# Kernel tuning notes

Measured on AMD Instinct MI355X. Metric: run time of the kernel, lower is better.

## Reference

```python
import jax, jax.numpy as jnp
import numpy as np

B, S, E, H = 4, 2048, 512, 8
D = E // H


def setup_inputs() -> dict:
    key = jax.random.key(0)
    ks = jax.random.split(key, 12)
    sc = 0.02
    return {
        "x": jax.random.normal(ks[0], (B, S, E), jnp.float32),
        "edge_bias": jax.random.normal(ks[1], (B, S, S), jnp.float32),
        "attn_mask": jax.random.randint(ks[2], (B, 1, S, S), 0, 2, jnp.int32),
        "Wq": jax.random.normal(ks[3], (E, E), jnp.float32) * sc,
        "bq": jnp.zeros((E,), jnp.float32),
        "Wk": jax.random.normal(ks[4], (E, E), jnp.float32) * sc,
        "bk": jnp.zeros((E,), jnp.float32),
        "Wv": jax.random.normal(ks[5], (E, E), jnp.float32) * sc,
        "bv": jnp.zeros((E,), jnp.float32),
        "Wo": jax.random.normal(ks[6], (E, E), jnp.float32) * sc,
        "bo": jnp.zeros((E,), jnp.float32),
    }


def reference(x, edge_bias, attn_mask, Wq, bq, Wk, bk, Wv, bv, Wo, bo):
    scale = D ** -0.5
    # projections -> [B, H, S, D]
    def proj(W, b):
        return (x @ W.T + b).reshape(B, S, H, D).transpose(0, 2, 1, 3)
    q = proj(Wq, bq)
    k = proj(Wk, bk)
    v = proj(Wv, bv)
    # scores [B, H, S, S] with edge bias and mask before softmax
    scores = jnp.einsum("bhqd,bhkd->bhqk", q, k) * scale
    scores = scores + edge_bias[:, None, :, :]
    scores = jnp.where(attn_mask == 0, -jnp.inf, scores)
    probs = jax.nn.softmax(scores, axis=-1)
    out = jnp.einsum("bhqk,bhkd->bhqd", probs, v)
    out = out.transpose(0, 2, 1, 3).reshape(B, S, E)
    return out @ Wo.T + bo
```

## Files before the change

### kernel.cpp

```cpp
#include <hip/hip_runtime.h>
#include <hip/hip_bf16.h>
#include <stdint.h>

#define DEV static __device__ __forceinline__

typedef float f32x4 __attribute__((ext_vector_type(4)));
typedef int   i32x4 __attribute__((ext_vector_type(4)));
typedef unsigned short u16x4 __attribute__((ext_vector_type(4)));
typedef unsigned u32x2 __attribute__((ext_vector_type(2)));
typedef unsigned u32x4 __attribute__((ext_vector_type(4)));
typedef __bf16 bf16x8 __attribute__((ext_vector_type(8)));

constexpr int Bb = 4, Ss = 2048, Ee = 512, Hh = 8, Dd = 64;
constexpr float LOG2E = 1.4426950408889634f;

DEV unsigned short f2bf(float f) {
  unsigned u = __float_as_uint(f);
  u += 0x7fff + ((u >> 16) & 1);
  return (unsigned short)(u >> 16);
}

DEV unsigned cvtpk(float lo, float hi) {
  unsigned r;
  asm("v_cvt_pk_bf16_f32 %0, %1, %2" : "=v"(r) : "v"(lo), "v"(hi));
  return r;
}

DEV void gload16(const void* g, void* l) {
  __builtin_amdgcn_global_load_lds((__attribute__((address_space(1))) void*)(g),
                                   (__attribute__((address_space(3))) void*)(l), 16, 0, 0);
}

__global__ void k_cvt(const float* __restrict__ src, unsigned short* __restrict__ dst, int n4) {
  int i = blockIdx.x * 256 + threadIdx.x;
  if (i >= n4) return;
  f32x4 v = *(const f32x4*)(src + (size_t)i * 4);
  u16x4 o;
#pragma unroll
  for (int j = 0; j < 4; ++j) o[j] = f2bf(v[j]);
  *(u16x4*)(dst + (size_t)i * 4) = o;
}

__global__ void k_mb(const float* __restrict__ bias, const int* __restrict__ mask,
                     unsigned short* __restrict__ mb, int n4) {
  int i = blockIdx.x * 256 + threadIdx.x;
  if (i >= n4) return;
  f32x4 v = *(const f32x4*)(bias + (size_t)i * 4);
  i32x4 m = *(const i32x4*)(mask + (size_t)i * 4);
  u16x4 o;
  const unsigned short NEG = f2bf(-1e38f * LOG2E);
#pragma unroll
  for (int j = 0; j < 4; ++j) o[j] = m[j] ? f2bf(v[j] * LOG2E) : NEG;
  *(u16x4*)(mb + (size_t)i * 4) = o;
}

template <int MODE>
__global__ __launch_bounds__(256) void k_gemm(
    const unsigned short* __restrict__ A, const unsigned short* __restrict__ Bw,
    const float* __restrict__ b0, const float* __restrict__ b1, const float* __restrict__ b2,
    unsigned short* __restrict__ oq, unsigned short* __restrict__ ok,
    unsigned short* __restrict__ ovt, float* __restrict__ of32) {
  __shared__ unsigned short Asl[128 * 32];
  __shared__ unsigned short Bsl[128 * 32];
  const int tid = threadIdx.x;
  const int wave = tid >> 6, lane = tid & 63;
  const int l15 = lane & 15, lg = lane >> 4;
  const int brow = blockIdx.x, bcol = blockIdx.y;
  const int wm = (wave >> 1) * 64, wn = (wave & 1) * 64;

  f32x4 acc[4][4] = {};

  for (int k0 = 0; k0 < 512; k0 += 32) {
    __syncthreads();
#pragma unroll
    for (int rnd = 0; rnd < 2; ++rnd) {
      int vid = rnd * 256 + tid;
      int r = vid >> 2, c = vid & 3;
      gload16(A + (size_t)(brow * 128 + r) * 512 + k0 + c * 8,
              Asl + (size_t)(rnd * 256 + wave * 64) * 8);
      gload16(Bw + (size_t)(bcol * 128 + r) * 512 + k0 + c * 8,
              Bsl + (size_t)(rnd * 256 + wave * 64) * 8);
    }
    __syncthreads();
    bf16x8 af[4], bfr[4];
#pragma unroll
    for (int m = 0; m < 4; ++m) af[m] = *(const bf16x8*)(Asl + (wm + m * 16 + l15) * 32 + lg * 8);
#pragma unroll
    for (int n = 0; n < 4; ++n) bfr[n] = *(const bf16x8*)(Bsl + (wn + n * 16 + l15) * 32 + lg * 8);
#pragma unroll
    for (int m = 0; m < 4; ++m)
#pragma unroll
      for (int n = 0; n < 4; ++n)
        acc[m][n] = __builtin_amdgcn_mfma_f32_16x16x32_bf16(af[m], bfr[n], acc[m][n], 0, 0, 0);
  }

  if (MODE == 0) {
    const int Nbase = bcol * 128;
    const int mat = Nbase >> 9;
    const int colb = Nbase & 511;
    const float* bp = (mat == 0) ? b0 : ((mat == 1) ? b1 : b2);
#pragma unroll
    for (int m = 0; m < 4; ++m)
#pragma unroll
      for (int n = 0; n < 4; ++n) {
        const int col = colb + wn + n * 16 + l15;
        const int h = col >> 6, d = col & 63;
        const float bv = bp[col];
#pragma unroll
        for (int j = 0; j < 4; ++j) {
          const int M = brow * 128 + wm + m * 16 + lg * 4 + j;
          const int b = M >> 11, s = M & 2047;
          float outv = acc[m][n][j] + bv;
          if (mat == 0) outv *= 0.125f * LOG2E;
          const unsigned short hv = f2bf(outv);
          if (mat == 0)
            oq[(((size_t)(b * Hh + h)) * Ss + s) * Dd + d] = hv;
          else if (mat == 1)
            ok[(((size_t)(b * Hh + h)) * Ss + s) * Dd + d] = hv;
          else
            ovt[(((size_t)(b * Hh + h)) * Dd + d) * Ss + s] = hv;
        }
      }
  } else {
#pragma unroll
    for (int m = 0; m < 4; ++m)
#pragma unroll
      for (int n = 0; n < 4; ++n) {
        const int col = bcol * 128 + wn + n * 16 + l15;
        const float bv = b0[col];
#pragma unroll
        for (int j = 0; j < 4; ++j) {
          const int M = brow * 128 + wm + m * 16 + lg * 4 + j;
          of32[(size_t)M * 512 + col] = acc[m][n][j] + bv;
        }
      }
  }
}

__global__ __launch_bounds__(256, 2) void k_attn(
    const unsigned short* __restrict__ q, const unsigned short* __restrict__ k,
    const unsigned short* __restrict__ vt, const unsigned short* __restrict__ mb,
    unsigned short* __restrict__ att) {
  __shared__ unsigned short Ksl[2][4096];
  __shared__ unsigned short Vsl[2][4096];
  __shared__ unsigned short Psl[4][2][1024];
  const int tid = threadIdx.x;
  const int wave = tid >> 6, lane = tid & 63;
  const int l15 = lane & 15, lg = lane >> 4;
  const int bid = blockIdx.x;
  const int xcd = bid & 7, slot = bid >> 3;
  const int bh = (xcd << 2) | (slot >> 4);
  const int qt = slot & 15;
  const int b = bh >> 3, h = bh & 7;
  const size_t qkb = (size_t)bh * Ss * Dd;
  const size_t vtbase = (size_t)bh * Dd * Ss;
  const int q0 = qt * 128 + wave * 32;

  const int swz = (l15 & 7) << 3;
  const int lgs8 = (lg ^ ((l15 >> 1) & 3)) * 8;

  bf16x8 qf[2][2];
#pragma unroll
  for (int g = 0; g < 2; ++g)
#pragma unroll
    for (int ks = 0; ks < 2; ++ks)
      qf[g][ks] = *(const bf16x8*)(q + qkb + (size_t)(q0 + g * 16 + l15) * Dd + ks * 32 + lg * 8);

  size_t mbrow[2];
#pragma unroll
  for (int g = 0; g < 2; ++g)
    mbrow[g] = ((size_t)b * Ss + (q0 + g * 16 + l15)) * Ss + lg * 4;

  const unsigned one2 = 0x3F803F80u;
  u32x4 ow; ow[0] = one2; ow[1] = one2; ow[2] = one2; ow[3] = one2;
  const bf16x8 onesv = __builtin_bit_cast(bf16x8, ow);

  f32x4 accO[2][4] = {};
  f32x4 accL[2] = {};

  {
#pragma unroll
    for (int rnd = 0; rnd < 2; ++rnd) {
      int v2 = rnd * 256 + tid;
      int ks = v2 >> 8, r = (v2 >> 2) & 63, c = v2 & 3;
      int cs = c ^ ((r >> 1) & 3);
      gload16(k + qkb + (size_t)r * Dd + ks * 32 + cs * 8,
              &Ksl[0][(rnd * 256 + wave * 64) * 8]);
    }
#pragma unroll
    for (int rnd = 0; rnd < 2; ++rnd) {
      int v2 = rnd * 256 + tid;
      int ks = v2 >> 8, r = (v2 >> 2) & 63, c = v2 & 3;
      int cs = c ^ ((r >> 1) & 3);
      gload16(vt + vtbase + (size_t)r * Ss + ks * 32 + cs * 8,
              &Vsl[0][(rnd * 256 + wave * 64) * 8]);
    }
  }
  u16x4 bvv[2][4];
#pragma unroll
  for (int g = 0; g < 2; ++g)
#pragma unroll
    for (int m = 0; m < 4; ++m)
      bvv[g][m] = *(const u16x4*)(mb + mbrow[g] + m * 16);

  for (int t = 0; t < 32; ++t) {
    const int cur = t & 1;
    __syncthreads();

    f32x4 binit[2][4];
#pragma unroll
    for (int g = 0; g < 2; ++g)
#pragma unroll
      for (int m = 0; m < 4; ++m)
#pragma unroll
        for (int j = 0; j < 4; ++j)
          binit[g][m][j] = __uint_as_float(((unsigned)bvv[g][m][j]) << 16);

    if (t < 31) {
      const int key0 = (t + 1) * 64;
#pragma unroll
      for (int rnd = 0; rnd < 2; ++rnd) {
        int v2 = rnd * 256 + tid;
        int ks = v2 >> 8, r = (v2 >> 2) & 63, c = v2 & 3;
        int cs = c ^ ((r >> 1) & 3);
        gload16(k + qkb + (size_t)(key0 + r) * Dd + ks * 32 + cs * 8,
                &Ksl[cur ^ 1][(rnd * 256 + wave * 64) * 8]);
      }
#pragma unroll
      for (int rnd = 0; rnd < 2; ++rnd) {
        int v2 = rnd * 256 + tid;
        int ks = v2 >> 8, r = (v2 >> 2) & 63, c = v2 & 3;
        int cs = c ^ ((r >> 1) & 3);
        gload16(vt + vtbase + (size_t)r * Ss + key0 + ks * 32 + cs * 8,
                &Vsl[cur ^ 1][(rnd * 256 + wave * 64) * 8]);
      }
#pragma unroll
      for (int g = 0; g < 2; ++g)
#pragma unroll
        for (int m = 0; m < 4; ++m)
          bvv[g][m] = *(const u16x4*)(mb + mbrow[g] + key0 + m * 16);
    }

    f32x4 sc[2][4];
    {
      bf16x8 kfm[4];
#pragma unroll
      for (int m = 0; m < 4; ++m)
        kfm[m] = *(const bf16x8*)(&Ksl[cur][(m * 16 + l15) * 32 + lgs8]);
      __builtin_amdgcn_s_setprio(1);
#pragma unroll
      for (int g = 0; g < 2; ++g)
#pragma unroll
        for (int m = 0; m < 4; ++m)
          sc[g][m] = __builtin_amdgcn_mfma_f32_16x16x32_bf16(kfm[m], qf[g][0], binit[g][m], 0, 0, 0);
      __builtin_amdgcn_s_setprio(0);
#pragma unroll
      for (int m = 0; m < 4; ++m)
        kfm[m] = *(const bf16x8*)(&Ksl[cur][2048 + (m * 16 + l15) * 32 + lgs8]);
      __builtin_amdgcn_s_setprio(1);
#pragma unroll
      for (int g = 0; g < 2; ++g)
#pragma unroll
        for (int m = 0; m < 4; ++m)
          sc[g][m] = __builtin_amdgcn_mfma_f32_16x16x32_bf16(kfm[m], qf[g][1], sc[g][m], 0, 0, 0);
      __builtin_amdgcn_s_setprio(0);
    }

#pragma unroll
    for (int m = 0; m < 4; ++m)
#pragma unroll
      for (int j = 0; j < 4; ++j) {
        sc[0][m][j] = exp2f(sc[0][m][j]);
        sc[1][m][j] = exp2f(sc[1][m][j]);
      }

#pragma unroll
    for (int g = 0; g < 2; ++g)
#pragma unroll
      for (int m = 0; m < 4; ++m) {
        u32x2 w;
        w[0] = cvtpk(sc[g][m][0], sc[g][m][1]);
        w[1] = cvtpk(sc[g][m][2], sc[g][m][3]);
        *(u32x2*)(&Psl[wave][g][(l15 * 64 + m * 16 + lg * 4) ^ swz]) = w;
      }
    asm volatile("" ::: "memory");

#pragma unroll
    for (int ks2 = 0; ks2 < 2; ++ks2) {
      bf16x8 va[4];
#pragma unroll
      for (int n = 0; n < 4; ++n)
        va[n] = *(const bf16x8*)(&Vsl[cur][ks2 * 2048 + (n * 16 + l15) * 32 + lgs8]);
      const bf16x8 pB0 = *(const bf16x8*)(&Psl[wave][0][(l15 * 64 + ks2 * 32 + lg * 8) ^ swz]);
      const bf16x8 pB1 = *(const bf16x8*)(&Psl[wave][1][(l15 * 64 + ks2 * 32 + lg * 8) ^ swz]);
      __builtin_amdgcn_s_setprio(1);
#pragma unroll
      for (int n = 0; n < 4; ++n) {
        accO[0][n] = __builtin_amdgcn_mfma_f32_16x16x32_bf16(va[n], pB0, accO[0][n], 0, 0, 0);
        accO[1][n] = __builtin_amdgcn_mfma_f32_16x16x32_bf16(va[n], pB1, accO[1][n], 0, 0, 0);
      }
      accL[0] = __builtin_amdgcn_mfma_f32_16x16x32_bf16(onesv, pB0, accL[0], 0, 0, 0);
      accL[1] = __builtin_amdgcn_mfma_f32_16x16x32_bf16(onesv, pB1, accL[1], 0, 0, 0);
      __builtin_amdgcn_s_setprio(0);
    }
  }

#pragma unroll
  for (int g = 0; g < 2; ++g) {
    const float invl = 1.0f / accL[g][0];
    const int qrow = q0 + g * 16 + l15;
#pragma unroll
    for (int n = 0; n < 4; ++n) {
      u16x4 o;
#pragma unroll
      for (int j = 0; j < 4; ++j) o[j] = f2bf(accO[g][n][j] * invl);
      *(u16x4*)(att + ((size_t)b * Ss + qrow) * Ee + h * Dd + n * 16 + lg * 4) = o;
    }
  }
}

extern "C" void kernel_launch(void* const* d_in, const int* in_sizes, int n_in,
                              void* d_out, int out_size, void* d_ws, size_t ws_size,
                              hipStream_t stream) {
  const float* x  = (const float*)d_in[0];
  const float* eb = (const float*)d_in[1];
  const int*   am = (const int*)d_in[2];
  const float* Wq = (const float*)d_in[3];
  const float* bq = (const float*)d_in[4];
  const float* Wk = (const float*)d_in[5];
  const float* bk = (const float*)d_in[6];
  const float* Wv = (const float*)d_in[7];
  const float* bv = (const float*)d_in[8];
  const float* Wo = (const float*)d_in[9];
  const float* bo = (const float*)d_in[10];
  float* out = (float*)d_out;

  unsigned short* xb   = (unsigned short*)d_ws;
  unsigned short* wqkv = xb + (size_t)8192 * 512;
  unsigned short* wo   = wqkv + (size_t)1536 * 512;
  unsigned short* qb   = wo + (size_t)512 * 512;
  unsigned short* kb   = qb + (size_t)Bb * Hh * Ss * Dd;
  unsigned short* vtb  = kb + (size_t)Bb * Hh * Ss * Dd;
  unsigned short* attb = vtb + (size_t)Bb * Hh * Ss * Dd;
  unsigned short* mbb  = attb + (size_t)8192 * 512;

  k_cvt<<<4096, 256, 0, stream>>>(x, xb, 8192 * 512 / 4);
  k_cvt<<<256, 256, 0, stream>>>(Wq, wqkv, 512 * 512 / 4);
  k_cvt<<<256, 256, 0, stream>>>(Wk, wqkv + (size_t)512 * 512, 512 * 512 / 4);
  k_cvt<<<256, 256, 0, stream>>>(Wv, wqkv + (size_t)1024 * 512, 512 * 512 / 4);
  k_cvt<<<256, 256, 0, stream>>>(Wo, wo, 512 * 512 / 4);
  k_mb<<<16384, 256, 0, stream>>>(eb, am, mbb, Bb * Ss * Ss / 4);

  dim3 blk(256);
  dim3 g1(64, 12);
  k_gemm<0><<<g1, blk, 0, stream>>>(xb, wqkv, bq, bk, bv, qb, kb, vtb, nullptr);
  k_attn<<<512, blk, 0, stream>>>(qb, kb, vtb, mbb, attb);
  dim3 g3(64, 4);
  k_gemm<1><<<g3, blk, 0, stream>>>(attb, wo, bo, nullptr, nullptr, nullptr, nullptr, nullptr, out);
}
```

Measured before the change: 165.2 us.

## Split attention over key halves with atomic fp32 reduction and separate normalize kernel

Attention blocks are doubled (1024) by splitting the key range into two halves per query tile. Partial unnormalized outputs and row sums go to fp32 workspace through atomics, and a new transpose/normalize kernel then writes the bf16 attention output. P staging in LDS is halved by processing the two query groups one after another, and launch bounds are raised to 4 blocks per CU for more occupancy. The cost is zeroing kernels, atomic traffic with a strided layout, and an extra pass over a 16MB fp32 buffer.

```diff
diff --git a/kernel.cpp b/kernel.cpp
--- a/kernel.cpp
+++ b/kernel.cpp
@@ -7,6 +7,7 @@
 typedef float f32x4 __attribute__((ext_vector_type(4)));
 typedef int   i32x4 __attribute__((ext_vector_type(4)));
 typedef unsigned short u16x4 __attribute__((ext_vector_type(4)));
+typedef unsigned short u16x8 __attribute__((ext_vector_type(8)));
 typedef unsigned u32x2 __attribute__((ext_vector_type(2)));
 typedef unsigned u32x4 __attribute__((ext_vector_type(4)));
 typedef __bf16 bf16x8 __attribute__((ext_vector_type(8)));
@@ -39,6 +40,13 @@
 #pragma unroll
   for (int j = 0; j < 4; ++j) o[j] = f2bf(v[j]);
   *(u16x4*)(dst + (size_t)i * 4) = o;
+}
+
+__global__ void k_zero(float* __restrict__ p, int n4) {
+  int i = blockIdx.x * 256 + threadIdx.x;
+  if (i >= n4) return;
+  f32x4 z = {};
+  *(f32x4*)(p + (size_t)i * 4) = z;
 }
 
 __global__ void k_mb(const float* __restrict__ bias, const int* __restrict__ mask,
@@ -137,24 +145,27 @@
   }
 }
 
-__global__ __launch_bounds__(256, 2) void k_attn(
+__global__ __launch_bounds__(256, 4) void k_attn(
     const unsigned short* __restrict__ q, const unsigned short* __restrict__ k,
     const unsigned short* __restrict__ vt, const unsigned short* __restrict__ mb,
-    unsigned short* __restrict__ att) {
+    float* __restrict__ accOf, float* __restrict__ accLf) {
   __shared__ unsigned short Ksl[2][4096];
   __shared__ unsigned short Vsl[2][4096];
-  __shared__ unsigned short Psl[4][2][1024];
+  __shared__ unsigned short Psl[4][1024];
   const int tid = threadIdx.x;
   const int wave = tid >> 6, lane = tid & 63;
   const int l15 = lane & 15, lg = lane >> 4;
   const int bid = blockIdx.x;
   const int xcd = bid & 7, slot = bid >> 3;
-  const int bh = (xcd << 2) | (slot >> 4);
-  const int qt = slot & 15;
+  const int bh = (xcd << 2) | (slot >> 5);
+  const int rem = slot & 31;
+  const int qt = rem >> 1;
+  const int ksp = rem & 1;
   const int b = bh >> 3, h = bh & 7;
   const size_t qkb = (size_t)bh * Ss * Dd;
   const size_t vtbase = (size_t)bh * Dd * Ss;
   const int q0 = qt * 128 + wave * 32;
+  const int kbase = ksp * 1024;
 
   const int swz = (l15 & 7) << 3;
   const int lgs8 = (lg ^ ((l15 >> 1) & 3)) * 8;
@@ -169,7 +180,7 @@
   size_t mbrow[2];
 #pragma unroll
   for (int g = 0; g < 2; ++g)
-    mbrow[g] = ((size_t)b * Ss + (q0 + g * 16 + l15)) * Ss + lg * 4;
+    mbrow[g] = ((size_t)b * Ss + (q0 + g * 16 + l15)) * Ss + lg * 4 + kbase;
 
   const unsigned one2 = 0x3F803F80u;
   u32x4 ow; ow[0] = one2; ow[1] = one2; ow[2] = one2; ow[3] = one2;
@@ -184,7 +195,7 @@
       int v2 = rnd * 256 + tid;
       int ks = v2 >> 8, r = (v2 >> 2) & 63, c = v2 & 3;
       int cs = c ^ ((r >> 1) & 3);
-      gload16(k + qkb + (size_t)r * Dd + ks * 32 + cs * 8,
+      gload16(k + qkb + (size_t)(kbase + r) * Dd + ks * 32 + cs * 8,
               &Ksl[0][(rnd * 256 + wave * 64) * 8]);
     }
 #pragma unroll
@@ -192,7 +203,7 @@
       int v2 = rnd * 256 + tid;
       int ks = v2 >> 8, r = (v2 >> 2) & 63, c = v2 & 3;
       int cs = c ^ ((r >> 1) & 3);
-      gload16(vt + vtbase + (size_t)r * Ss + ks * 32 + cs * 8,
+      gload16(vt + vtbase + (size_t)r * Ss + kbase + ks * 32 + cs * 8,
               &Vsl[0][(rnd * 256 + wave * 64) * 8]);
     }
   }
@@ -203,7 +214,7 @@
     for (int m = 0; m < 4; ++m)
       bvv[g][m] = *(const u16x4*)(mb + mbrow[g] + m * 16);
 
-  for (int t = 0; t < 32; ++t) {
+  for (int t = 0; t < 16; ++t) {
     const int cur = t & 1;
     __syncthreads();
 
@@ -216,8 +227,8 @@
         for (int j = 0; j < 4; ++j)
           binit[g][m][j] = __uint_as_float(((unsigned)bvv[g][m][j]) << 16);
 
-    if (t < 31) {
-      const int key0 = (t + 1) * 64;
+    if (t < 15) {
+      const int key0 = kbase + (t + 1) * 64;
 #pragma unroll
       for (int rnd = 0; rnd < 2; ++rnd) {
         int v2 = rnd * 256 + tid;
@@ -238,7 +249,7 @@
       for (int g = 0; g < 2; ++g)
 #pragma unroll
         for (int m = 0; m < 4; ++m)
-          bvv[g][m] = *(const u16x4*)(mb + mbrow[g] + key0 + m * 16);
+          bvv[g][m] = *(const u16x4*)(mb + mbrow[g] + (t + 1) * 64 + m * 16);
     }
 
     f32x4 sc[2][4];
@@ -274,48 +285,98 @@
         sc[1][m][j] = exp2f(sc[1][m][j]);
       }
 
-#pragma unroll
-    for (int g = 0; g < 2; ++g)
-#pragma unroll
-      for (int m = 0; m < 4; ++m) {
-        u32x2 w;
-        w[0] = cvtpk(sc[g][m][0], sc[g][m][1]);
-        w[1] = cvtpk(sc[g][m][2], sc[g][m][3]);
-        *(u32x2*)(&Psl[wave][g][(l15 * 64 + m * 16 + lg * 4) ^ swz]) = w;
-      }
+    bf16x8 va[2][4];
+#pragma unroll
+    for (int ks2 = 0; ks2 < 2; ++ks2)
+#pragma unroll
+      for (int n = 0; n < 4; ++n)
+        va[ks2][n] = *(const bf16x8*)(&Vsl[cur][ks2 * 2048 + (n * 16 + l15) * 32 + lgs8]);
+
+#pragma unroll
+    for (int m = 0; m < 4; ++m) {
+      u32x2 w;
+      w[0] = cvtpk(sc[0][m][0], sc[0][m][1]);
+      w[1] = cvtpk(sc[0][m][2], sc[0][m][3]);
+      *(u32x2*)(&Psl[wave][(l15 * 64 + m * 16 + lg * 4) ^ swz]) = w;
+    }
     asm volatile("" ::: "memory");
-
 #pragma unroll
     for (int ks2 = 0; ks2 < 2; ++ks2) {
-      bf16x8 va[4];
+      const bf16x8 pB = *(const bf16x8*)(&Psl[wave][(l15 * 64 + ks2 * 32 + lg * 8) ^ swz]);
+      __builtin_amdgcn_s_setprio(1);
 #pragma unroll
       for (int n = 0; n < 4; ++n)
-        va[n] = *(const bf16x8*)(&Vsl[cur][ks2 * 2048 + (n * 16 + l15) * 32 + lgs8]);
-      const bf16x8 pB0 = *(const bf16x8*)(&Psl[wave][0][(l15 * 64 + ks2 * 32 + lg * 8) ^ swz]);
-      const bf16x8 pB1 = *(const bf16x8*)(&Psl[wave][1][(l15 * 64 + ks2 * 32 + lg * 8) ^ swz]);
+        accO[0][n] = __builtin_amdgcn_mfma_f32_16x16x32_bf16(va[ks2][n], pB, accO[0][n], 0, 0, 0);
+      accL[0] = __builtin_amdgcn_mfma_f32_16x16x32_bf16(onesv, pB, accL[0], 0, 0, 0);
+      __builtin_amdgcn_s_setprio(0);
+    }
+    asm volatile("" ::: "memory");
+
+#pragma unroll
+    for (int m = 0; m < 4; ++m) {
+      u32x2 w;
+      w[0] = cvtpk(sc[1][m][0], sc[1][m][1]);
+      w[1] = cvtpk(sc[1][m][2], sc[1][m][3]);
+      *(u32x2*)(&Psl[wave][(l15 * 64 + m * 16 + lg * 4) ^ swz]) = w;
+    }
+    asm volatile("" ::: "memory");
+#pragma unroll
+    for (int ks2 = 0; ks2 < 2; ++ks2) {
+      const bf16x8 pB = *(const bf16x8*)(&Psl[wave][(l15 * 64 + ks2 * 32 + lg * 8) ^ swz]);
       __builtin_amdgcn_s_setprio(1);
 #pragma unroll
-      for (int n = 0; n < 4; ++n) {
-        accO[0][n] = __builtin_amdgcn_mfma_f32_16x16x32_bf16(va[n], pB0, accO[0][n], 0, 0, 0);
-        accO[1][n] = __builtin_amdgcn_mfma_f32_16x16x32_bf16(va[n], pB1, accO[1][n], 0, 0, 0);
-      }
-      accL[0] = __builtin_amdgcn_mfma_f32_16x16x32_bf16(onesv, pB0, accL[0], 0, 0, 0);
-      accL[1] = __builtin_amdgcn_mfma_f32_16x16x32_bf16(onesv, pB1, accL[1], 0, 0, 0);
+      for (int n = 0; n < 4; ++n)
+        accO[1][n] = __builtin_amdgcn_mfma_f32_16x16x32_bf16(va[ks2][n], pB, accO[1][n], 0, 0, 0);
+      accL[1] = __builtin_amdgcn_mfma_f32_16x16x32_bf16(onesv, pB, accL[1], 0, 0, 0);
       __builtin_amdgcn_s_setprio(0);
     }
   }
 
 #pragma unroll
   for (int g = 0; g < 2; ++g) {
-    const float invl = 1.0f / accL[g][0];
     const int qrow = q0 + g * 16 + l15;
 #pragma unroll
-    for (int n = 0; n < 4; ++n) {
-      u16x4 o;
-#pragma unroll
-      for (int j = 0; j < 4; ++j) o[j] = f2bf(accO[g][n][j] * invl);
-      *(u16x4*)(att + ((size_t)b * Ss + qrow) * Ee + h * Dd + n * 16 + lg * 4) = o;
-    }
+    for (int n = 0; n < 4; ++n)
+#pragma unroll
+      for (int j = 0; j < 4; ++j) {
+        const int d = n * 16 + lg * 4 + j;
+        unsafeAtomicAdd(&accOf[((size_t)bh * Dd + d) * Ss + qrow], accO[g][n][j]);
+      }
+    if (lg == 0)
+      unsafeAtomicAdd(&accLf[(size_t)bh * Ss + qrow], accL[g][0]);
+  }
+}
+
+__global__ __launch_bounds__(256) void k_norm(const float* __restrict__ accOf,
+                                              const float* __restrict__ accLf,
+                                              unsigned short* __restrict__ att) {
+  __shared__ float tile[64][129];
+  __shared__ float Lrow[128];
+  const int tid = threadIdx.x;
+  const int bh = blockIdx.x >> 4;
+  const int sc0 = (blockIdx.x & 15) * 128;
+  const int b = bh >> 3, h = bh & 7;
+
+#pragma unroll
+  for (int i = 0; i < 8; ++i) {
+    int idx = i * 256 + tid;
+    int d = idx >> 5, sq = idx & 31;
+    f32x4 v = *(const f32x4*)(accOf + ((size_t)bh * 64 + d) * Ss + sc0 + sq * 4);
+#pragma unroll
+    for (int e = 0; e < 4; ++e) tile[d][sq * 4 + e] = v[e];
+  }
+  if (tid < 128) Lrow[tid] = accLf[(size_t)bh * Ss + sc0 + tid];
+  __syncthreads();
+
+#pragma unroll
+  for (int i = 0; i < 4; ++i) {
+    int idx = i * 256 + tid;
+    int s_loc = idx >> 3, dc = idx & 7;
+    const float invl = 1.0f / Lrow[s_loc];
+    u16x8 o;
+#pragma unroll
+    for (int e = 0; e < 8; ++e) o[e] = f2bf(tile[dc * 8 + e][s_loc] * invl);
+    *(u16x8*)(att + ((size_t)b * Ss + sc0 + s_loc) * Ee + h * Dd + dc * 8) = o;
   }
 }
 
@@ -343,18 +404,23 @@
   unsigned short* vtb  = kb + (size_t)Bb * Hh * Ss * Dd;
   unsigned short* attb = vtb + (size_t)Bb * Hh * Ss * Dd;
   unsigned short* mbb  = attb + (size_t)8192 * 512;
+  float* accOf = (float*)(mbb + (size_t)Bb * Ss * Ss);
+  float* accLf = accOf + (size_t)32 * 64 * 2048;
 
   k_cvt<<<4096, 256, 0, stream>>>(x, xb, 8192 * 512 / 4);
   k_cvt<<<256, 256, 0, stream>>>(Wq, wqkv, 512 * 512 / 4);
   k_cvt<<<256, 256, 0, stream>>>(Wk, wqkv + (size_t)512 * 512, 512 * 512 / 4);
   k_cvt<<<256, 256, 0, stream>>>(Wv, wqkv + (size_t)1024 * 512, 512 * 512 / 4);
   k_cvt<<<256, 256, 0, stream>>>(Wo, wo, 512 * 512 / 4);
+  k_zero<<<4096, 256, 0, stream>>>(accOf, 32 * 64 * 2048 / 4);
+  k_zero<<<64, 256, 0, stream>>>(accLf, 32 * 2048 / 4);
   k_mb<<<16384, 256, 0, stream>>>(eb, am, mbb, Bb * Ss * Ss / 4);
 
   dim3 blk(256);
   dim3 g1(64, 12);
   k_gemm<0><<<g1, blk, 0, stream>>>(xb, wqkv, bq, bk, bv, qb, kb, vtb, nullptr);
-  k_attn<<<512, blk, 0, stream>>>(qb, kb, vtb, mbb, attb);
+  k_attn<<<1024, blk, 0, stream>>>(qb, kb, vtb, mbb, accOf, accLf);
+  k_norm<<<512, blk, 0, stream>>>(accOf, accLf, attb);
   dim3 g3(64, 4);
   k_gemm<1><<<g3, blk, 0, stream>>>(attb, wo, bo, nullptr, nullptr, nullptr, nullptr, nullptr, out);
 }
```

Measured after the change: 264.0 us. 59.8% more time.
